# Performance work log

Measured on AMD Instinct MI355X. Metric: run time of the kernel, lower is better.

## Reference

```python
import jax, jax.numpy as jnp
import numpy as np

DIM = 1024
NUM_HEADS = 16
HEAD_DIM = DIM // NUM_HEADS
SCALE = HEAD_DIM ** -0.5
HIDDEN = int(DIM * 1.0)


def setup_inputs() -> dict:
    key = jax.random.key(0)
    ks = jax.random.split(key, 11)
    s = 0.02
    return {
        "x":  jax.random.normal(ks[0], (2, 2048, DIM), jnp.float32),
        "Wq": jax.random.normal(ks[1], (DIM, DIM), jnp.float32) * s,
        "bq": jnp.zeros((DIM,), jnp.float32),
        "Wk": jax.random.normal(ks[2], (DIM, DIM), jnp.float32) * s,
        "bk": jnp.zeros((DIM,), jnp.float32),
        "Wv": jax.random.normal(ks[3], (DIM, DIM), jnp.float32) * s,
        "bv": jnp.zeros((DIM,), jnp.float32),
        "W1": jax.random.normal(ks[4], (HIDDEN, DIM), jnp.float32) * s,
        "b1": jnp.zeros((HIDDEN,), jnp.float32),
        "W2": jax.random.normal(ks[5], (DIM, HIDDEN), jnp.float32) * s,
        "b2": jnp.zeros((DIM,), jnp.float32),
    }


def _split_heads(t, B, S):
    # [B,S,C] -> [B,H,S,hd]
    return t.reshape(B, S, NUM_HEADS, HEAD_DIM).transpose(0, 2, 1, 3)


def reference(x, Wq, bq, Wk, bk, Wv, bv, W1, b1, W2, b2):
    B, S, C = x.shape
    q = _split_heads(x @ Wq.T + bq, B, S) * SCALE
    k = _split_heads(x @ Wk.T + bk, B, S)
    v = _split_heads(x @ Wv.T + bv, B, S)
    # softmax-free bilinear attention, scores in float32 (matches .float())
    attn = jnp.einsum('bhqd,bhkd->bhqk', q.astype(jnp.float32), k.astype(jnp.float32))
    out = jnp.einsum('bhqk,bhkd->bhqd', attn, v)  # [B,H,S,hd]
    out = out.transpose(0, 2, 1, 3).reshape(B, S, C)
    h = jax.nn.gelu(out @ W1.T + b1, approximate=False)
    mlp = h @ W2.T + b2
    return x + out + mlp
```

## Files before the change

### kernel.cpp

```cpp
#include <hip/hip_runtime.h>
#include <math.h>

#define DIM    1024
#define BATCH  2
#define SEQ    2048
#define NHEAD  16
#define HDIM   64
#define MROWS  (BATCH*SEQ)
#define NSPLIT 8

typedef unsigned short u16;
typedef __attribute__((ext_vector_type(8))) short  s16x8;
typedef __attribute__((ext_vector_type(4))) float  f32x4;

__device__ __forceinline__ float bf2f(u16 h) {
    unsigned u = ((unsigned)h) << 16; float f; __builtin_memcpy(&f, &u, 4); return f;
}
__device__ __forceinline__ u16 f2bf(float f) {
    unsigned u; __builtin_memcpy(&u, &f, 4);
    u += 0x7FFFu + ((u >> 16) & 1u);
    return (u16)(u >> 16);
}

__device__ __forceinline__ void glds16(const u16* g, u16* l) {
    __builtin_amdgcn_global_load_lds(
        (const __attribute__((address_space(1))) void*)g,
        (__attribute__((address_space(3))) void*)l, 16, 0, 0);
}

__global__ __launch_bounds__(256)
void pack_all(const float* __restrict__ x,
              const float* __restrict__ Wq, const float* __restrict__ Wk,
              const float* __restrict__ Wv, const float* __restrict__ W1,
              const float* __restrict__ W2,
              u16* __restrict__ xb, u16* __restrict__ Wqb, u16* __restrict__ Wkb,
              u16* __restrict__ Wvb, u16* __restrict__ W1b, u16* __restrict__ W2b)
{
    const int bid = blockIdx.x;
    const float* src; u16* dst; int i;
    if (bid < 4096) { src = x; dst = xb; i = bid * 256 + threadIdx.x; }
    else {
        const int w = (bid - 4096) >> 10;
        const int lb = (bid - 4096) & 1023;
        src = (w == 0) ? Wq : (w == 1) ? Wk : (w == 2) ? Wv : (w == 3) ? W1 : W2;
        dst = (w == 0) ? Wqb : (w == 1) ? Wkb : (w == 2) ? Wvb : (w == 3) ? W1b : W2b;
        i = lb * 256 + threadIdx.x;
    }
    float4 v = ((const float4*)src)[i];
    ushort4 o = { f2bf(v.x), f2bf(v.y), f2bf(v.z), f2bf(v.w) };
    ((ushort4*)dst)[i] = o;
}

__device__ __forceinline__ void gemm_core_pf128(const u16* __restrict__ Ab,
                                                const u16* __restrict__ Bb,
                                                u16* As, u16* Bs,
                                                int tid, f32x4 acc[4][4])
{
    const int w = tid >> 6, l = tid & 63;
    const int wm = (w >> 1) * 64, wn = (w & 1) * 64;
    const int lr = l & 15, kq = l >> 4;

    const int srow = w * 16 + (l >> 2);
    const int scol = (((l & 3) ^ ((srow >> 1) & 3)) << 3);
    const u16* gA = Ab + (size_t)srow * DIM + scol;
    const u16* gB = Bb + (size_t)srow * DIM + scol;
    const int sdst = w * 512;

    glds16(gA,      As + sdst);         glds16(gA + 64 * DIM,      As + 2048 + sdst);
    glds16(gB,      Bs + sdst);         glds16(gB + 64 * DIM,      Bs + 2048 + sdst);
    glds16(gA + 32, As + 4096 + sdst);  glds16(gA + 32 + 64 * DIM, As + 4096 + 2048 + sdst);
    glds16(gB + 32, Bs + 4096 + sdst);  glds16(gB + 32 + 64 * DIM, Bs + 4096 + 2048 + sdst);

    const int NIT = DIM / 32;
    int cur = 0, nxt2 = 2;
    for (int it = 0; it < NIT; ++it) {
        if (it < NIT - 1) { asm volatile("s_waitcnt vmcnt(4)" ::: "memory"); }
        else              { asm volatile("s_waitcnt vmcnt(0)" ::: "memory"); }
        __builtin_amdgcn_s_barrier();
        asm volatile("" ::: "memory");
        if (it + 2 < NIT) {
            const int k = (it + 2) * 32;
            u16* An = As + nxt2 * 4096 + sdst;
            u16* Bn = Bs + nxt2 * 4096 + sdst;
            glds16(gA + k, An);  glds16(gA + k + 64 * DIM, An + 2048);
            glds16(gB + k, Bn);  glds16(gB + k + 64 * DIM, Bn + 2048);
        }
        const u16* Ac = As + cur * 4096;
        const u16* Bc = Bs + cur * 4096;
        s16x8 af[4], bfr[4];
        #pragma unroll
        for (int i = 0; i < 4; ++i) {
            const int ra = wm + i * 16 + lr;
            af[i]  = *(const s16x8*)(Ac + ra * 32 + ((kq ^ ((ra >> 1) & 3)) << 3));
        }
        #pragma unroll
        for (int j = 0; j < 4; ++j) {
            const int rb = wn + j * 16 + lr;
            bfr[j] = *(const s16x8*)(Bc + rb * 32 + ((kq ^ ((rb >> 1) & 3)) << 3));
        }
        __builtin_amdgcn_s_setprio(1);
        #pragma unroll
        for (int i = 0; i < 4; ++i)
            #pragma unroll
            for (int j = 0; j < 4; ++j)
                acc[i][j] = __builtin_amdgcn_mfma_f32_16x16x32_bf16(af[i], bfr[j], acc[i][j], 0, 0, 0);
        __builtin_amdgcn_s_setprio(0);
        cur  = (cur  == 2) ? 0 : cur  + 1;
        nxt2 = (nxt2 == 2) ? 0 : nxt2 + 1;
    }
}

__device__ __forceinline__ void gemm_core_pf64(const u16* __restrict__ Ab,
                                               const u16* __restrict__ Bb,
                                               u16* As , u16* Bs ,
                                               int tid, f32x4 acc[2][4])
{
    const int w  = tid >> 6, l = tid & 63;
    const int wm = (w >> 1) * 32, wn = (w & 1) * 64;
    const int lr = l & 15, kq = l >> 4;

    const int srow = w * 16 + (l >> 2);
    const int scol = (((l & 3) ^ ((srow >> 1) & 3)) << 3);
    const u16* gA = Ab + (size_t)srow * DIM + scol;
    const u16* gB = Bb + (size_t)srow * DIM + scol;
    const int sdst = w * 512;

    glds16(gA,      As + sdst);
    glds16(gB,      Bs + sdst);        glds16(gB + 64 * DIM,      Bs + 2048 + sdst);
    glds16(gA + 32, As + 2048 + sdst);
    glds16(gB + 32, Bs + 4096 + sdst); glds16(gB + 32 + 64 * DIM, Bs + 4096 + 2048 + sdst);

    const int NIT = DIM / 32;
    int cur = 0, nxt2 = 2;
    for (int it = 0; it < NIT; ++it) {
        if (it < NIT - 1) { asm volatile("s_waitcnt vmcnt(3)" ::: "memory"); }
        else              { asm volatile("s_waitcnt vmcnt(0)" ::: "memory"); }
        __builtin_amdgcn_s_barrier();
        asm volatile("" ::: "memory");
        if (it + 2 < NIT) {
            const int k = (it + 2) * 32;
            u16* An = As + nxt2 * 2048 + sdst;
            u16* Bn = Bs + nxt2 * 4096 + sdst;
            glds16(gA + k, An);
            glds16(gB + k, Bn);  glds16(gB + k + 64 * DIM, Bn + 2048);
        }
        const u16* Ac = As + cur * 2048;
        const u16* Bc = Bs + cur * 4096;
        s16x8 af[2], bfr[4];
        #pragma unroll
        for (int i = 0; i < 2; ++i) {
            const int ra = wm + i * 16 + lr;
            af[i]  = *(const s16x8*)(Ac + ra * 32 + ((kq ^ ((ra >> 1) & 3)) << 3));
        }
        #pragma unroll
        for (int j = 0; j < 4; ++j) {
            const int rb = wn + j * 16 + lr;
            bfr[j] = *(const s16x8*)(Bc + rb * 32 + ((kq ^ ((rb >> 1) & 3)) << 3));
        }
        __builtin_amdgcn_s_setprio(1);
        #pragma unroll
        for (int i = 0; i < 2; ++i)
            #pragma unroll
            for (int j = 0; j < 4; ++j)
                acc[i][j] = __builtin_amdgcn_mfma_f32_16x16x32_bf16(af[i], bfr[j], acc[i][j], 0, 0, 0);
        __builtin_amdgcn_s_setprio(0);
        cur  = (cur  == 2) ? 0 : cur  + 1;
        nxt2 = (nxt2 == 2) ? 0 : nxt2 + 1;
    }
}

__global__ __launch_bounds__(256)
void qkv_gemm(const u16* __restrict__ xb,
              const u16* __restrict__ Wq, const u16* __restrict__ Wk, const u16* __restrict__ Wv,
              const float* __restrict__ bq, const float* __restrict__ bk, const float* __restrict__ bv,
              u16* __restrict__ qo, u16* __restrict__ ko, u16* __restrict__ vo)
{
    __shared__ __align__(16) u16 SH[24576];
    const int tid = threadIdx.x;
    const int m0  = blockIdx.x * 128;
    const int sel = blockIdx.y >> 3;
    const int n0  = (blockIdx.y & 7) * 128;
    const u16*   B    = (sel == 0) ? Wq : (sel == 1) ? Wk : Wv;
    const float* bias = (sel == 0) ? bq : (sel == 1) ? bk : bv;
    u16*         C    = (sel == 0) ? qo : (sel == 1) ? ko : vo;
    const float scale = (sel == 0) ? 0.125f : 1.0f;

    f32x4 acc[4][4];
    #pragma unroll
    for (int i = 0; i < 4; ++i)
        #pragma unroll
        for (int j = 0; j < 4; ++j) acc[i][j] = (f32x4){0.f, 0.f, 0.f, 0.f};

    gemm_core_pf128(xb + (size_t)m0 * DIM, B + (size_t)n0 * DIM, SH, SH + 12288, tid, acc);

    __syncthreads();
    const int w = tid >> 6, l = tid & 63;
    const int wm = (w >> 1) * 64, wn = (w & 1) * 64;
    const int er = l >> 4, ec = l & 15;
    #pragma unroll
    for (int j = 0; j < 4; ++j) {
        const int colv = wn + j * 16 + ec;
        const float bb = bias[n0 + colv];
        const int cg = colv >> 3, cl = colv & 7;
        #pragma unroll
        for (int i = 0; i < 4; ++i)
            #pragma unroll
            for (int r = 0; r < 4; ++r) {
                const int row = wm + i * 16 + er * 4 + r;
                const int g = ((row >> 2) & 3) << 1;
                SH[row * 128 + ((cg ^ g) << 3) + cl] = f2bf((acc[i][j][r] + bb) * scale);
            }
    }
    __syncthreads();
    {
        const int cg = tid & 15, rr = tid >> 4;
        #pragma unroll
        for (int pass = 0; pass < 8; ++pass) {
            const int row = rr + (pass << 4);
            const int g = ((row >> 2) & 3) << 1;
            uint4 v = *(const uint4*)(SH + row * 128 + ((cg ^ g) << 3));
            *(uint4*)(C + (size_t)(m0 + row) * DIM + n0 + (cg << 3)) = v;
        }
    }
}

__global__ __launch_bounds__(256, 2)
void gemm_bf16(const u16* __restrict__ A, const u16* __restrict__ B,
               const float* __restrict__ bias,
               u16* __restrict__ Cb, float* __restrict__ Cf,
               const float* __restrict__ rx, const u16* __restrict__ rattn,
               int mode)
{
    __shared__ __align__(16) u16 SH[18432];
    const int tid = threadIdx.x;
    const int m0 = blockIdx.x * 64, n0 = blockIdx.y * 128;

    f32x4 acc[2][4];
    #pragma unroll
    for (int i = 0; i < 2; ++i)
        #pragma unroll
        for (int j = 0; j < 4; ++j) acc[i][j] = (f32x4){0.f, 0.f, 0.f, 0.f};

    gemm_core_pf64(A + (size_t)m0 * DIM, B + (size_t)n0 * DIM, SH, SH + 6144, tid, acc);

    const int w = tid >> 6, l = tid & 63;
    const int wm = (w >> 1) * 32, wn = (w & 1) * 64;
    const int er = l >> 4, ec = l & 15;

    if (mode == 1) {
        __syncthreads();
        #pragma unroll
        for (int j = 0; j < 4; ++j) {
            const int colv = wn + j * 16 + ec;
            const float bb = bias[n0 + colv];
            const int cg = colv >> 3, cl = colv & 7;
            #pragma unroll
            for (int i = 0; i < 2; ++i)
                #pragma unroll
                for (int r = 0; r < 4; ++r) {
                    const int row = wm + i * 16 + er * 4 + r;
                    const int g = ((row >> 2) & 3) << 1;
                    float v = acc[i][j][r] + bb;
                    v = 0.5f * v * (1.0f + erff(v * 0.70710678118654752f));
                    SH[row * 128 + ((cg ^ g) << 3) + cl] = f2bf(v);
                }
        }
        __syncthreads();
        const int cg = tid & 15, rr = tid >> 4;
        #pragma unroll
        for (int pass = 0; pass < 4; ++pass) {
            const int row = rr + (pass << 4);
            const int g = ((row >> 2) & 3) << 1;
            uint4 v = *(const uint4*)(SH + row * 128 + ((cg ^ g) << 3));
            *(uint4*)(Cb + (size_t)(m0 + row) * DIM + n0 + (cg << 3)) = v;
        }
    } else {
        float* SHF = (float*)SH;
        #pragma unroll
        for (int h = 0; h < 2; ++h) {
            __syncthreads();
            if ((w >> 1) == h) {
                #pragma unroll
                for (int j = 0; j < 4; ++j) {
                    const int colv = wn + j * 16 + ec;
                    const float bb = bias[n0 + colv];
                    const int c4 = colv >> 2, c2 = colv & 3;
                    #pragma unroll
                    for (int i = 0; i < 2; ++i)
                        #pragma unroll
                        for (int r = 0; r < 4; ++r) {
                            const int rl = i * 16 + er * 4 + r;
                            const int g4 = ((rl >> 2) & 1) << 2;
                            SHF[rl * 128 + ((c4 ^ g4) << 2) + c2] = acc[i][j][r] + bb;
                        }
                }
            }
            __syncthreads();
            const int c4 = tid & 31, rr = tid >> 5;
            #pragma unroll
            for (int pass = 0; pass < 4; ++pass) {
                const int rl = rr + (pass << 3);
                const int g4 = ((rl >> 2) & 1) << 2;
                float4 v = *(const float4*)(SHF + rl * 128 + ((c4 ^ g4) << 2));
                const size_t idx = (size_t)(m0 + 32 * h + rl) * DIM + n0 + (c4 << 2);
                float4 rxv = *(const float4*)(rx + idx);
                ushort4 rav = *(const ushort4*)(rattn + idx);
                float4 o = { v.x + rxv.x + bf2f(rav.x),
                             v.y + rxv.y + bf2f(rav.y),
                             v.z + rxv.z + bf2f(rav.z),
                             v.w + rxv.w + bf2f(rav.w) };
                *(float4*)(Cf + idx) = o;
            }
        }
    }
}

__global__ __launch_bounds__(256)
void ktv_mfma(const u16* __restrict__ Kb, const u16* __restrict__ Vb,
              float* __restrict__ part)
{
    __shared__ u16 Kt[64 * 264];
    __shared__ u16 Vt[64 * 264];
    const int tid = threadIdx.x;
    const int bh = blockIdx.x & 31;
    const int sp = blockIdx.x >> 5;
    const int b = bh >> 4, h = bh & 15;
    const size_t base = (size_t)b * SEQ * DIM + (size_t)h * HDIM + (size_t)sp * 256 * DIM;

    const int dg = (tid & 15) * 4;
    #pragma unroll
    for (int pass = 0; pass < 16; ++pass) {
        const int s = (tid >> 4) + 16 * pass;
        ushort4 kv = *(const ushort4*)(Kb + base + (size_t)s * DIM + dg);
        ushort4 vv = *(const ushort4*)(Vb + base + (size_t)s * DIM + dg);
        Kt[(dg + 0) * 264 + s] = kv.x; Kt[(dg + 1) * 264 + s] = kv.y;
        Kt[(dg + 2) * 264 + s] = kv.z; Kt[(dg + 3) * 264 + s] = kv.w;
        Vt[(dg + 0) * 264 + s] = vv.x; Vt[(dg + 1) * 264 + s] = vv.y;
        Vt[(dg + 2) * 264 + s] = vv.z; Vt[(dg + 3) * 264 + s] = vv.w;
    }
    __syncthreads();

    const int w = tid >> 6, l = tid & 63;
    const int lr = l & 15, kq = l >> 4;
    f32x4 acc[4];
    #pragma unroll
    for (int j = 0; j < 4; ++j) acc[j] = (f32x4){0.f, 0.f, 0.f, 0.f};

    for (int k0 = 0; k0 < 256; k0 += 32) {
        s16x8 af = *(const s16x8*)(Kt + (w * 16 + lr) * 264 + k0 + kq * 8);
        #pragma unroll
        for (int j = 0; j < 4; ++j) {
            s16x8 bf = *(const s16x8*)(Vt + (j * 16 + lr) * 264 + k0 + kq * 8);
            acc[j] = __builtin_amdgcn_mfma_f32_16x16x32_bf16(af, bf, acc[j], 0, 0, 0);
        }
    }

    float* dst = part + ((size_t)sp * 32 + bh) * (HDIM * HDIM);
    const int er = l >> 4, ec = l & 15;
    #pragma unroll
    for (int j = 0; j < 4; ++j)
        #pragma unroll
        for (int r = 0; r < 4; ++r)
            dst[(w * 16 + er * 4 + r) * HDIM + j * 16 + ec] = acc[j][r];
}

__global__ __launch_bounds__(256)
void qktv_kernel(const u16* __restrict__ Qb, const float* __restrict__ part,
                 u16* __restrict__ attnb)
{
    __shared__ float KV[HDIM * HDIM];
    __shared__ u16 Qs[128 * 68];
    const int tid = threadIdx.x;
    const int h  = blockIdx.x;
    const int mt = blockIdx.y;
    const int row0 = mt * 128;
    const int b = row0 >> 11;
    const int bh = b * NHEAD + h;

    for (int i = tid; i < HDIM * HDIM; i += 256) {
        float s = 0.f;
        #pragma unroll
        for (int sp = 0; sp < NSPLIT; ++sp)
            s += part[((size_t)sp * 32 + bh) * (HDIM * HDIM) + i];
        KV[i] = s;
    }
    const int dg = (tid & 15) * 4;
    #pragma unroll
    for (int pass = 0; pass < 8; ++pass) {
        const int r = (tid >> 4) + 16 * pass;
        ushort4 q = *(const ushort4*)(Qb + (size_t)(row0 + r) * DIM + h * HDIM + dg);
        *(ushort4*)(Qs + r * 68 + dg) = q;
    }
    __syncthreads();

    const int tr = tid >> 3, tc = tid & 7;
    const int r0 = tr * 4, c0 = tc * 8;
    float acc[4][8] = {};
    for (int d = 0; d < HDIM; ++d) {
        float4 ka  = *(const float4*)&KV[d * HDIM + c0];
        float4 kb2 = *(const float4*)&KV[d * HDIM + c0 + 4];
        const float* k8a = (const float*)&ka;
        const float* k8b = (const float*)&kb2;
        float qv[4];
        #pragma unroll
        for (int i = 0; i < 4; ++i) qv[i] = bf2f(Qs[(r0 + i) * 68 + d]);
        #pragma unroll
        for (int i = 0; i < 4; ++i)
            #pragma unroll
            for (int j = 0; j < 4; ++j) {
                acc[i][j]     += qv[i] * k8a[j];
                acc[i][j + 4] += qv[i] * k8b[j];
            }
    }
    #pragma unroll
    for (int i = 0; i < 4; ++i) {
        u16* dst = attnb + (size_t)(row0 + r0 + i) * DIM + h * HDIM + c0;
        ushort4 o0 = { f2bf(acc[i][0]), f2bf(acc[i][1]), f2bf(acc[i][2]), f2bf(acc[i][3]) };
        ushort4 o1 = { f2bf(acc[i][4]), f2bf(acc[i][5]), f2bf(acc[i][6]), f2bf(acc[i][7]) };
        *(ushort4*)(dst)     = o0;
        *(ushort4*)(dst + 4) = o1;
    }
}

extern "C" void kernel_launch(void* const* d_in, const int* in_sizes, int n_in,
                              void* d_out, int out_size, void* d_ws, size_t ws_size,
                              hipStream_t stream)
{
    const float* x  = (const float*)d_in[0];
    const float* Wq = (const float*)d_in[1];
    const float* bq = (const float*)d_in[2];
    const float* Wk = (const float*)d_in[3];
    const float* bk = (const float*)d_in[4];
    const float* Wv = (const float*)d_in[5];
    const float* bv = (const float*)d_in[6];
    const float* W1 = (const float*)d_in[7];
    const float* b1 = (const float*)d_in[8];
    const float* W2 = (const float*)d_in[9];
    const float* b2 = (const float*)d_in[10];
    float* out = (float*)d_out;

    char* ws = (char*)d_ws;
    const size_t MB = 1u << 20;
    u16* xb   = (u16*)(ws);
    u16* Wqb  = (u16*)(ws +  8 * MB);
    u16* Wkb  = (u16*)(ws + 10 * MB);
    u16* Wvb  = (u16*)(ws + 12 * MB);
    u16* W1b  = (u16*)(ws + 14 * MB);
    u16* W2b  = (u16*)(ws + 16 * MB);
    u16* qb   = (u16*)(ws + 18 * MB);
    u16* kb   = (u16*)(ws + 26 * MB);
    u16* vb   = (u16*)(ws + 34 * MB);
    float* part = (float*)(ws + 42 * MB);
    u16* attnb = kb;
    u16* h1b   = vb;

    pack_all<<<4096 + 5 * 1024, 256, 0, stream>>>(x, Wq, Wk, Wv, W1, W2,
                                                  xb, Wqb, Wkb, Wvb, W1b, W2b);

    qkv_gemm<<<dim3(32, 24), 256, 0, stream>>>(xb, Wqb, Wkb, Wvb, bq, bk, bv, qb, kb, vb);

    ktv_mfma<<<NSPLIT * 32, 256, 0, stream>>>(kb, vb, part);
    qktv_kernel<<<dim3(NHEAD, MROWS / 128), 256, 0, stream>>>(qb, part, attnb);

    gemm_bf16<<<dim3(64, 8), 256, 0, stream>>>(attnb, W1b, b1, h1b, nullptr, nullptr, nullptr, 1);
    gemm_bf16<<<dim3(64, 8), 256, 0, stream>>>(h1b, W2b, b2, nullptr, out, x, attnb, 2);
}
```

Before: 189.8 us.

## Use single-wave 32x64 tiles for MLP GEMMs without block barriers

The MLP GEMMs move from 256-thread blocks with 64x128 tiles to 64-thread single-wave blocks with 32x64 tiles, launched as a 128x16 grid. Because one wave owns its whole LDS tile, all s_barrier and __syncthreads calls are removed, and the epilogue uses padded rows instead of XOR swizzles. This is meant to remove barrier stalls and raise the number of blocks available to fill the CUs. In exchange each wave reloads more A and B data per output (less reuse), there are many more small blocks, and the padded LDS layout may cause bank conflicts.

```diff
diff --git a/kernel.cpp b/kernel.cpp
--- a/kernel.cpp
+++ b/kernel.cpp
@@ -110,65 +110,6 @@
     }
 }
 
-__device__ __forceinline__ void gemm_core_pf64(const u16* __restrict__ Ab,
-                                               const u16* __restrict__ Bb,
-                                               u16* As , u16* Bs ,
-                                               int tid, f32x4 acc[2][4])
-{
-    const int w  = tid >> 6, l = tid & 63;
-    const int wm = (w >> 1) * 32, wn = (w & 1) * 64;
-    const int lr = l & 15, kq = l >> 4;
-
-    const int srow = w * 16 + (l >> 2);
-    const int scol = (((l & 3) ^ ((srow >> 1) & 3)) << 3);
-    const u16* gA = Ab + (size_t)srow * DIM + scol;
-    const u16* gB = Bb + (size_t)srow * DIM + scol;
-    const int sdst = w * 512;
-
-    glds16(gA,      As + sdst);
-    glds16(gB,      Bs + sdst);        glds16(gB + 64 * DIM,      Bs + 2048 + sdst);
-    glds16(gA + 32, As + 2048 + sdst);
-    glds16(gB + 32, Bs + 4096 + sdst); glds16(gB + 32 + 64 * DIM, Bs + 4096 + 2048 + sdst);
-
-    const int NIT = DIM / 32;
-    int cur = 0, nxt2 = 2;
-    for (int it = 0; it < NIT; ++it) {
-        if (it < NIT - 1) { asm volatile("s_waitcnt vmcnt(3)" ::: "memory"); }
-        else              { asm volatile("s_waitcnt vmcnt(0)" ::: "memory"); }
-        __builtin_amdgcn_s_barrier();
-        asm volatile("" ::: "memory");
-        if (it + 2 < NIT) {
-            const int k = (it + 2) * 32;
-            u16* An = As + nxt2 * 2048 + sdst;
-            u16* Bn = Bs + nxt2 * 4096 + sdst;
-            glds16(gA + k, An);
-            glds16(gB + k, Bn);  glds16(gB + k + 64 * DIM, Bn + 2048);
-        }
-        const u16* Ac = As + cur * 2048;
-        const u16* Bc = Bs + cur * 4096;
-        s16x8 af[2], bfr[4];
-        #pragma unroll
-        for (int i = 0; i < 2; ++i) {
-            const int ra = wm + i * 16 + lr;
-            af[i]  = *(const s16x8*)(Ac + ra * 32 + ((kq ^ ((ra >> 1) & 3)) << 3));
-        }
-        #pragma unroll
-        for (int j = 0; j < 4; ++j) {
-            const int rb = wn + j * 16 + lr;
-            bfr[j] = *(const s16x8*)(Bc + rb * 32 + ((kq ^ ((rb >> 1) & 3)) << 3));
-        }
-        __builtin_amdgcn_s_setprio(1);
-        #pragma unroll
-        for (int i = 0; i < 2; ++i)
-            #pragma unroll
-            for (int j = 0; j < 4; ++j)
-                acc[i][j] = __builtin_amdgcn_mfma_f32_16x16x32_bf16(af[i], bfr[j], acc[i][j], 0, 0, 0);
-        __builtin_amdgcn_s_setprio(0);
-        cur  = (cur  == 2) ? 0 : cur  + 1;
-        nxt2 = (nxt2 == 2) ? 0 : nxt2 + 1;
-    }
-}
-
 __global__ __launch_bounds__(256)
 void qkv_gemm(const u16* __restrict__ xb,
               const u16* __restrict__ Wq, const u16* __restrict__ Wk, const u16* __restrict__ Wv,
@@ -224,16 +165,25 @@
     }
 }
 
-__global__ __launch_bounds__(256, 2)
+__global__ __launch_bounds__(64)
 void gemm_bf16(const u16* __restrict__ A, const u16* __restrict__ B,
                const float* __restrict__ bias,
                u16* __restrict__ Cb, float* __restrict__ Cf,
                const float* __restrict__ rx, const u16* __restrict__ rattn,
                int mode)
 {
-    __shared__ __align__(16) u16 SH[18432];
-    const int tid = threadIdx.x;
-    const int m0 = blockIdx.x * 64, n0 = blockIdx.y * 128;
+    __shared__ __align__(16) u16 SH[9216];
+    const int l = threadIdx.x;
+    const int m0 = blockIdx.x * 32, n0 = blockIdx.y * 64;
+    const int lr = l & 15, kq = l >> 4;
+
+    u16* As = SH;
+    u16* Bs = SH + 3072;
+
+    const int srow = l >> 2;
+    const int scol = (((l & 3) ^ ((l >> 3) & 3)) << 3);
+    const u16* gA = A + (size_t)(m0 + srow) * DIM + scol;
+    const u16* gB = B + (size_t)(n0 + srow) * DIM + scol;
 
     f32x4 acc[2][4];
     #pragma unroll
@@ -241,76 +191,104 @@
         #pragma unroll
         for (int j = 0; j < 4; ++j) acc[i][j] = (f32x4){0.f, 0.f, 0.f, 0.f};
 
-    gemm_core_pf64(A + (size_t)m0 * DIM, B + (size_t)n0 * DIM, SH, SH + 6144, tid, acc);
-
-    const int w = tid >> 6, l = tid & 63;
-    const int wm = (w >> 1) * 32, wn = (w & 1) * 64;
+    #pragma unroll
+    for (int t = 0; t < 2; ++t) {
+        const int k = t * 32;
+        glds16(gA + k,            As + t * 1024);
+        glds16(gA + k + 16 * DIM, As + t * 1024 + 512);
+        glds16(gB + k,            Bs + t * 2048);
+        glds16(gB + k + 16 * DIM, Bs + t * 2048 + 512);
+        glds16(gB + k + 32 * DIM, Bs + t * 2048 + 1024);
+        glds16(gB + k + 48 * DIM, Bs + t * 2048 + 1536);
+    }
+
+    const int rdo = lr * 32 + ((kq ^ ((lr >> 1) & 3)) << 3);
+
+    const int NIT = DIM / 32;
+    int cur = 0, nxt2 = 2;
+    for (int it = 0; it < NIT; ++it) {
+        if (it < NIT - 1) { asm volatile("s_waitcnt vmcnt(6)" ::: "memory"); }
+        else              { asm volatile("s_waitcnt vmcnt(0)" ::: "memory"); }
+        if (it + 2 < NIT) {
+            const int k = (it + 2) * 32;
+            u16* An = As + nxt2 * 1024;
+            u16* Bn = Bs + nxt2 * 2048;
+            glds16(gA + k,            An);
+            glds16(gA + k + 16 * DIM, An + 512);
+            glds16(gB + k,            Bn);
+            glds16(gB + k + 16 * DIM, Bn + 512);
+            glds16(gB + k + 32 * DIM, Bn + 1024);
+            glds16(gB + k + 48 * DIM, Bn + 1536);
+        }
+        const u16* Ac = As + cur * 1024;
+        const u16* Bc = Bs + cur * 2048;
+        s16x8 af[2], bfr[4];
+        #pragma unroll
+        for (int i = 0; i < 2; ++i)
+            af[i]  = *(const s16x8*)(Ac + i * 512 + rdo);
+        #pragma unroll
+        for (int j = 0; j < 4; ++j)
+            bfr[j] = *(const s16x8*)(Bc + j * 512 + rdo);
+        __builtin_amdgcn_s_setprio(1);
+        #pragma unroll
+        for (int i = 0; i < 2; ++i)
+            #pragma unroll
+            for (int j = 0; j < 4; ++j)
+                acc[i][j] = __builtin_amdgcn_mfma_f32_16x16x32_bf16(af[i], bfr[j], acc[i][j], 0, 0, 0);
+        __builtin_amdgcn_s_setprio(0);
+        cur  = (cur  == 2) ? 0 : cur  + 1;
+        nxt2 = (nxt2 == 2) ? 0 : nxt2 + 1;
+    }
+
     const int er = l >> 4, ec = l & 15;
-
     if (mode == 1) {
-        __syncthreads();
+        u16* SHW = SH;
         #pragma unroll
         for (int j = 0; j < 4; ++j) {
-            const int colv = wn + j * 16 + ec;
+            const int colv = j * 16 + ec;
             const float bb = bias[n0 + colv];
-            const int cg = colv >> 3, cl = colv & 7;
             #pragma unroll
             for (int i = 0; i < 2; ++i)
                 #pragma unroll
                 for (int r = 0; r < 4; ++r) {
-                    const int row = wm + i * 16 + er * 4 + r;
-                    const int g = ((row >> 2) & 3) << 1;
+                    const int row = i * 16 + er * 4 + r;
                     float v = acc[i][j][r] + bb;
                     v = 0.5f * v * (1.0f + erff(v * 0.70710678118654752f));
-                    SH[row * 128 + ((cg ^ g) << 3) + cl] = f2bf(v);
+                    SHW[row * 72 + colv] = f2bf(v);
                 }
         }
-        __syncthreads();
-        const int cg = tid & 15, rr = tid >> 4;
-        #pragma unroll
-        for (int pass = 0; pass < 4; ++pass) {
-            const int row = rr + (pass << 4);
-            const int g = ((row >> 2) & 3) << 1;
-            uint4 v = *(const uint4*)(SH + row * 128 + ((cg ^ g) << 3));
-            *(uint4*)(Cb + (size_t)(m0 + row) * DIM + n0 + (cg << 3)) = v;
-        }
+        const int row = l >> 1, half = l & 1;
+        const u16* srcp = SHW + row * 72 + half * 32;
+        u16* dst = Cb + (size_t)(m0 + row) * DIM + n0 + half * 32;
+        #pragma unroll
+        for (int q = 0; q < 4; ++q)
+            *(uint4*)(dst + q * 8) = *(const uint4*)(srcp + q * 8);
     } else {
         float* SHF = (float*)SH;
         #pragma unroll
-        for (int h = 0; h < 2; ++h) {
-            __syncthreads();
-            if ((w >> 1) == h) {
+        for (int j = 0; j < 4; ++j) {
+            const int colv = j * 16 + ec;
+            const float bb = bias[n0 + colv];
+            #pragma unroll
+            for (int i = 0; i < 2; ++i)
                 #pragma unroll
-                for (int j = 0; j < 4; ++j) {
-                    const int colv = wn + j * 16 + ec;
-                    const float bb = bias[n0 + colv];
-                    const int c4 = colv >> 2, c2 = colv & 3;
-                    #pragma unroll
-                    for (int i = 0; i < 2; ++i)
-                        #pragma unroll
-                        for (int r = 0; r < 4; ++r) {
-                            const int rl = i * 16 + er * 4 + r;
-                            const int g4 = ((rl >> 2) & 1) << 2;
-                            SHF[rl * 128 + ((c4 ^ g4) << 2) + c2] = acc[i][j][r] + bb;
-                        }
+                for (int r = 0; r < 4; ++r) {
+                    const int row = i * 16 + er * 4 + r;
+                    SHF[row * 72 + colv] = acc[i][j][r] + bb;
                 }
-            }
-            __syncthreads();
-            const int c4 = tid & 31, rr = tid >> 5;
-            #pragma unroll
-            for (int pass = 0; pass < 4; ++pass) {
-                const int rl = rr + (pass << 3);
-                const int g4 = ((rl >> 2) & 1) << 2;
-                float4 v = *(const float4*)(SHF + rl * 128 + ((c4 ^ g4) << 2));
-                const size_t idx = (size_t)(m0 + 32 * h + rl) * DIM + n0 + (c4 << 2);
-                float4 rxv = *(const float4*)(rx + idx);
-                ushort4 rav = *(const ushort4*)(rattn + idx);
-                float4 o = { v.x + rxv.x + bf2f(rav.x),
-                             v.y + rxv.y + bf2f(rav.y),
-                             v.z + rxv.z + bf2f(rav.z),
-                             v.w + rxv.w + bf2f(rav.w) };
-                *(float4*)(Cf + idx) = o;
-            }
+        }
+        const int row = l >> 1, half = l & 1;
+        #pragma unroll
+        for (int q = 0; q < 8; ++q) {
+            const size_t idx = (size_t)(m0 + row) * DIM + n0 + half * 32 + q * 4;
+            float4 v = *(const float4*)(SHF + row * 72 + half * 32 + q * 4);
+            float4 rxv = *(const float4*)(rx + idx);
+            ushort4 rav = *(const ushort4*)(rattn + idx);
+            float4 o = { v.x + rxv.x + bf2f(rav.x),
+                         v.y + rxv.y + bf2f(rav.y),
+                         v.z + rxv.z + bf2f(rav.z),
+                         v.w + rxv.w + bf2f(rav.w) };
+            *(float4*)(Cf + idx) = o;
         }
     }
 }
@@ -462,6 +440,6 @@
     ktv_mfma<<<NSPLIT * 32, 256, 0, stream>>>(kb, vb, part);
     qktv_kernel<<<dim3(NHEAD, MROWS / 128), 256, 0, stream>>>(qb, part, attnb);
 
-    gemm_bf16<<<dim3(64, 8), 256, 0, stream>>>(attnb, W1b, b1, h1b, nullptr, nullptr, nullptr, 1);
-    gemm_bf16<<<dim3(64, 8), 256, 0, stream>>>(h1b, W2b, b2, nullptr, out, x, attnb, 2);
-}
+    gemm_bf16<<<dim3(128, 16), 64, 0, stream>>>(attnb, W1b, b1, h1b, nullptr, nullptr, nullptr, 1);
+    gemm_bf16<<<dim3(128, 16), 64, 0, stream>>>(h1b, W2b, b2, nullptr, out, x, attnb, 2);
+}
```

New measurement: 215.9 us. 1.14x slower.
